# Optimization experiments

Hardware: AMD Instinct MI355X
Metric: run time of the kernel (lower is better)

## Reference

```python
import jax, jax.numpy as jnp
import numpy as np

B, C, N, K = 8, 128, 4096, 16
EPS = 1e-5


def _bn(x, g, b, m, v):
    # eval-mode BatchNorm1d over channel dim of [B, C, N]
    scale = (g * jax.lax.rsqrt(v + EPS))[None, :, None]
    return x * scale + (b - m * g * jax.lax.rsqrt(v + EPS))[None, :, None]


def setup_inputs() -> dict:
    key = jax.random.key(0)
    ks = jax.random.split(key, 16)
    x = jax.random.normal(ks[0], (B, C, N), dtype=jnp.float32)
    # k incoming neighbors per node, src within the same batch graph
    src_local = jax.random.randint(ks[1], (B, N, K), 0, N)
    src = (src_local + jnp.arange(B, dtype=src_local.dtype)[:, None, None] * N).reshape(B * N, K)
    def u(k, shape, lo, hi):
        return jax.random.uniform(k, shape, jnp.float32, lo, hi)
    params = dict(
        W1=jax.random.normal(ks[2], (C, C), jnp.float32) * (1.0 / np.sqrt(C)),
        b1=jax.random.normal(ks[3], (C,), jnp.float32) * 0.02,
        g1=u(ks[4], (C,), 0.5, 1.5), be1=jax.random.normal(ks[5], (C,)) * 0.1,
        m1=jax.random.normal(ks[6], (C,)) * 0.1, v1=u(ks[7], (C,), 0.5, 1.5),
        Wmr=jax.random.normal(ks[8], (2 * C, 2 * C), jnp.float32) * (1.0 / np.sqrt(2 * C)),
        bmr=jax.random.normal(ks[9], (2 * C,), jnp.float32) * 0.02,
        W2=jax.random.normal(ks[10], (C, 2 * C), jnp.float32) * (1.0 / np.sqrt(2 * C)),
        b2=jax.random.normal(ks[11], (C,), jnp.float32) * 0.02,
        g2=u(ks[12], (C,), 0.5, 1.5), be2=jax.random.normal(ks[13], (C,)) * 0.1,
        m2=jax.random.normal(ks[14], (C,)) * 0.1, v2=u(ks[15], (C,), 0.5, 1.5),
    )
    return {"x": x, "src": src, **params}


def reference(x, src, W1, b1, g1, be1, m1, v1, Wmr, bmr, W2, b2, g2, be2, m2, v2):
    res = x
    # fc1: Conv1d(k=1) + BN, then ReLU
    h = jnp.einsum('oc,bcn->bon', W1, x) + b1[None, :, None]
    h = jax.nn.relu(_bn(h, g1, be1, m1, v1))
    # nodes: [B*N, C]
    xn = h.transpose(0, 2, 1).reshape(B * N, C)
    # MRConv: max over incoming edges of (dst - src) feature diff
    diff = xn[:, None, :] - xn[src]          # [B*N, K, C]
    max_diff = diff.max(axis=1)              # [B*N, C]
    cat = jnp.concatenate([xn, max_diff], axis=1)  # [B*N, 2C]
    hn = jax.nn.relu(cat @ Wmr.T + bmr)      # [B*N, 2C]
    h2 = hn.reshape(B, N, 2 * C).transpose(0, 2, 1)  # [B, 2C, N]
    # fc2: Conv1d(k=1) + BN
    out = jnp.einsum('oc,bcn->bon', W2, h2) + b2[None, :, None]
    out = _bn(out, g2, be2, m2, v2)
    out = out + res
    return jax.nn.relu(out)
```

## Files before the change

### kernel.cpp

```cpp
#include <hip/hip_runtime.h>


typedef short bf8_t __attribute__((ext_vector_type(8)));
typedef float f4_t  __attribute__((ext_vector_type(4)));

namespace {
constexpr int Bn = 8, Cc = 128, Nn = 4096, Kk = 16, C2 = 256;
constexpr int NODES = Bn * Nn;
constexpr float EPSf = 1e-5f;
}

__device__ __forceinline__ unsigned short f2bf(float f) {
    unsigned u = __float_as_uint(f);
    u += 0x7fffu + ((u >> 16) & 1u);
    return (unsigned short)(u >> 16);
}
__device__ __forceinline__ unsigned pk2(float a, float b) {
    return (unsigned)f2bf(a) | ((unsigned)f2bf(b) << 16);
}
__device__ __forceinline__ float bflo(unsigned u) { return __uint_as_float(u << 16); }
__device__ __forceinline__ float bfhi(unsigned u) { return __uint_as_float(u & 0xffff0000u); }
__device__ __forceinline__ unsigned diff2(unsigned o, unsigned m) {
    return pk2(bflo(o) - bflo(m), bfhi(o) - bfhi(m));
}

__device__ __forceinline__ bf8_t cvt_frag(const float* __restrict__ p) {
    const float4 a = *(const float4*)(p);
    const float4 b = *(const float4*)(p + 4);
    union { uint4 u; bf8_t f; } r;
    r.u.x = pk2(a.x, a.y);
    r.u.y = pk2(a.z, a.w);
    r.u.z = pk2(b.x, b.y);
    r.u.w = pk2(b.z, b.w);
    return r.f;
}

#define PKMIN(a, b) asm("v_pk_min_u16 %0, %0, %1" : "+v"(a) : "v"(b))

__global__ __launch_bounds__(512) void fc1_mfma(
    const float* __restrict__ x, const float* __restrict__ W1,
    const float* __restrict__ b1, const float* __restrict__ g1,
    const float* __restrict__ be1, const float* __restrict__ m1,
    const float* __restrict__ v1, const float* __restrict__ Wmr,
    const float* __restrict__ W2, ushort* __restrict__ Wmrbf,
    ushort* __restrict__ W2bf, ushort* __restrict__ xn)
{
    __shared__ __align__(16) ushort xS[64 * 136];
    __shared__ float scS[Cc], shS[Cc];
    const int t = threadIdx.x;
    const int bid = blockIdx.x;

    if (bid < 96) {
        const int e = bid * 1024 + t * 2;
        if (e < 65536) {
            const float2 v = *(const float2*)(Wmr + e);
            *(unsigned*)(Wmrbf + e) = pk2(v.x, v.y);
        } else {
            const float2 v = *(const float2*)(W2 + (e - 65536));
            *(unsigned*)(W2bf + (e - 65536)) = pk2(v.x, v.y);
        }
    }

    const int lb = (bid & 7) * 64 + (bid >> 3);
    const int node0 = lb * 64;
    const int b  = node0 >> 12;
    const int n0 = node0 & 4095;

    if (t < Cc) {
        const float s = g1[t] * rsqrtf(v1[t] + EPSf);
        scS[t] = s;
        shS[t] = (b1[t] - m1[t]) * s + be1[t];
    }

    {
        const int cp = t >> 3, q = t & 7;
        const float* p0 = x + ((size_t)(b * Cc + 2 * cp)) * Nn + n0 + q * 8;
        const float* p1 = p0 + Nn;
        const float4 a0 = *(const float4*)(p0);
        const float4 a1 = *(const float4*)(p0 + 4);
        const float4 c0 = *(const float4*)(p1);
        const float4 c1 = *(const float4*)(p1 + 4);
        ushort* base = xS + (size_t)q * 8 * 136 + ((cp * 2) ^ (q << 3));
        *(unsigned*)(base + 0 * 136) = pk2(a0.x, c0.x);
        *(unsigned*)(base + 1 * 136) = pk2(a0.y, c0.y);
        *(unsigned*)(base + 2 * 136) = pk2(a0.z, c0.z);
        *(unsigned*)(base + 3 * 136) = pk2(a0.w, c0.w);
        *(unsigned*)(base + 4 * 136) = pk2(a1.x, c1.x);
        *(unsigned*)(base + 5 * 136) = pk2(a1.y, c1.y);
        *(unsigned*)(base + 6 * 136) = pk2(a1.z, c1.z);
        *(unsigned*)(base + 7 * 136) = pk2(a1.w, c1.w);
    }
    __syncthreads();

    const int w = t >> 6, lane = t & 63;
    const int row16 = lane & 15, kg = lane >> 4;

    f4_t acc[4];
    const f4_t zero = {0.f, 0.f, 0.f, 0.f};
    #pragma unroll
    for (int j = 0; j < 4; ++j) acc[j] = zero;

    #pragma unroll
    for (int ks = 0; ks < 4; ++ks) {
        const int k0 = ks * 32 + kg * 8;
        const bf8_t aw = cvt_frag(W1 + (size_t)(w * 16 + row16) * Cc + k0);
        #pragma unroll
        for (int nsub = 0; nsub < 4; ++nsub) {
            const int n = nsub * 16 + row16;
            const bf8_t bx = *(const bf8_t*)(xS + n * 136 + (k0 ^ ((n >> 3) << 3)));
            acc[nsub] = __builtin_amdgcn_mfma_f32_16x16x32_bf16(aw, bx, acc[nsub], 0, 0, 0);
        }
    }

    const int o4 = w * 16 + kg * 4;
    const float s0 = scS[o4 + 0], s1 = scS[o4 + 1], s2 = scS[o4 + 2], s3 = scS[o4 + 3];
    const float h0 = shS[o4 + 0], h1 = shS[o4 + 1], h2 = shS[o4 + 2], h3 = shS[o4 + 3];
    #pragma unroll
    for (int nsub = 0; nsub < 4; ++nsub) {
        const int node = node0 + nsub * 16 + row16;
        float v0 = acc[nsub][0] * s0 + h0;
        float v1 = acc[nsub][1] * s1 + h1;
        float v2 = acc[nsub][2] * s2 + h2;
        float v3 = acc[nsub][3] * s3 + h3;
        v0 = v0 > 0.f ? v0 : 0.f;
        v1 = v1 > 0.f ? v1 : 0.f;
        v2 = v2 > 0.f ? v2 : 0.f;
        v3 = v3 > 0.f ? v3 : 0.f;
        uint2 pk;
        pk.x = pk2(v0, v1);
        pk.y = pk2(v2, v3);
        *(uint2*)(xn + (size_t)node * Cc + o4) = pk;
    }
}

__global__ __launch_bounds__(512) void mrfc2_mfma(
    const ushort* __restrict__ xn, const int* __restrict__ src,
    const ushort* __restrict__ Wmrbf, const float* __restrict__ bmr,
    const ushort* __restrict__ W2bf, const float* __restrict__ x,
    const float* __restrict__ b2, const float* __restrict__ g2,
    const float* __restrict__ be2, const float* __restrict__ m2,
    const float* __restrict__ v2, float* __restrict__ out)
{
    __shared__ __align__(16) ushort catS[64 * 264];
    __shared__ __align__(16) float xresS[128 * 64];
    __shared__ float scS[Cc], shS[Cc];
    const int t = threadIdx.x;
    const int bid = blockIdx.x;
    const int lb = (bid & 7) * 64 + (bid >> 3);
    const int node0 = lb * 64;
    const int b  = node0 >> 12;
    const int n0 = node0 & 4095;

    const int xo = t >> 2, xseg = t & 3;
    const float* xsrc = x + ((size_t)(b * Cc + xo)) * Nn + n0 + xseg * 16;
    const float4 xr0 = ((const float4*)xsrc)[0];
    const float4 xr1 = ((const float4*)xsrc)[1];
    const float4 xr2 = ((const float4*)xsrc)[2];
    const float4 xr3 = ((const float4*)xsrc)[3];

    {
        const int nl = t >> 3, q = t & 7;
        const int node = node0 + nl;
        const int4 si0 = *(const int4*)(src + (size_t)node * Kk + 0);
        const int4 si1 = *(const int4*)(src + (size_t)node * Kk + 4);
        const int4 si2 = *(const int4*)(src + (size_t)node * Kk + 8);
        const int4 si3 = *(const int4*)(src + (size_t)node * Kk + 12);
        const int sl[16] = {si0.x, si0.y, si0.z, si0.w,
                            si1.x, si1.y, si1.z, si1.w,
                            si2.x, si2.y, si2.z, si2.w,
                            si3.x, si3.y, si3.z, si3.w};
        const ushort* orow = xn + (size_t)node * Cc + q * 16;
        uint4 ow0 = *(const uint4*)(orow + 0);
        uint4 ow1 = *(const uint4*)(orow + 8);
        const ushort* sr = xn + (size_t)sl[0] * Cc + q * 16;
        uint4 mn0 = *(const uint4*)(sr + 0);
        uint4 mn1 = *(const uint4*)(sr + 8);
        #pragma unroll
        for (int k = 1; k < Kk; ++k) {
            const ushort* s = xn + (size_t)sl[k] * Cc + q * 16;
            uint4 v0 = *(const uint4*)(s + 0);
            uint4 v1 = *(const uint4*)(s + 8);
            PKMIN(mn0.x, v0.x); PKMIN(mn0.y, v0.y); PKMIN(mn0.z, v0.z); PKMIN(mn0.w, v0.w);
            PKMIN(mn1.x, v1.x); PKMIN(mn1.y, v1.y); PKMIN(mn1.z, v1.z); PKMIN(mn1.w, v1.w);
        }
        unsigned* crow = (unsigned*)(catS + nl * 264);
        *(uint4*)(crow + q * 8 + 0) = ow0;
        *(uint4*)(crow + q * 8 + 4) = ow1;
        uint4 d0, d1;
        d0.x = diff2(ow0.x, mn0.x); d0.y = diff2(ow0.y, mn0.y);
        d0.z = diff2(ow0.z, mn0.z); d0.w = diff2(ow0.w, mn0.w);
        d1.x = diff2(ow1.x, mn1.x); d1.y = diff2(ow1.y, mn1.y);
        d1.z = diff2(ow1.z, mn1.z); d1.w = diff2(ow1.w, mn1.w);
        *(uint4*)(crow + 64 + q * 8 + 0) = d0;
        *(uint4*)(crow + 64 + q * 8 + 4) = d1;
    }

    {
        float* xd = xresS + xo * 64 + xseg * 16;
        ((float4*)xd)[0] = xr0;
        ((float4*)xd)[1] = xr1;
        ((float4*)xd)[2] = xr2;
        ((float4*)xd)[3] = xr3;
    }
    __syncthreads();

    const int w = t >> 6, lane = t & 63;
    const int row16 = lane & 15, kg = lane >> 4;

    const int jb = w * 32;
    {
        f4_t acc[2][4];
        const f4_t zero = {0.f, 0.f, 0.f, 0.f};
        #pragma unroll
        for (int i = 0; i < 2; ++i)
            #pragma unroll
            for (int j = 0; j < 4; ++j) acc[i][j] = zero;

        #pragma unroll
        for (int ks = 0; ks < 8; ++ks) {
            const int k0 = ks * 32 + kg * 8;
            bf8_t aw[2], bc[4];
            #pragma unroll
            for (int jsub = 0; jsub < 2; ++jsub)
                aw[jsub] = *(const bf8_t*)(Wmrbf + (size_t)(jb + jsub * 16 + row16) * C2 + k0);
            #pragma unroll
            for (int nsub = 0; nsub < 4; ++nsub)
                bc[nsub] = *(const bf8_t*)(catS + (nsub * 16 + row16) * 264 + k0);
            #pragma unroll
            for (int jsub = 0; jsub < 2; ++jsub)
                #pragma unroll
                for (int nsub = 0; nsub < 4; ++nsub)
                    acc[jsub][nsub] = __builtin_amdgcn_mfma_f32_16x16x32_bf16(
                        aw[jsub], bc[nsub], acc[jsub][nsub], 0, 0, 0);
        }

        if (t < Cc) {
            const float s = g2[t] * rsqrtf(v2[t] + EPSf);
            scS[t] = s;
            shS[t] = (b2[t] - m2[t]) * s + be2[t];
        }
        __syncthreads();

        #pragma unroll
        for (int jsub = 0; jsub < 2; ++jsub) {
            const float4 bb = *(const float4*)(bmr + jb + jsub * 16 + kg * 4);
            #pragma unroll
            for (int nsub = 0; nsub < 4; ++nsub) {
                float v0 = acc[jsub][nsub][0] + bb.x;
                float v1 = acc[jsub][nsub][1] + bb.y;
                float v2_ = acc[jsub][nsub][2] + bb.z;
                float v3 = acc[jsub][nsub][3] + bb.w;
                v0 = v0 > 0.f ? v0 : 0.f;
                v1 = v1 > 0.f ? v1 : 0.f;
                v2_ = v2_ > 0.f ? v2_ : 0.f;
                v3 = v3 > 0.f ? v3 : 0.f;
                uint2 pk;
                pk.x = pk2(v0, v1);
                pk.y = pk2(v2_, v3);
                *(uint2*)(catS + (nsub * 16 + row16) * 264 + jb + jsub * 16 + kg * 4) = pk;
            }
        }
    }
    __syncthreads();

    {
        const int ob = w * 16;
        f4_t acc[4];
        const f4_t zero = {0.f, 0.f, 0.f, 0.f};
        #pragma unroll
        for (int j = 0; j < 4; ++j) acc[j] = zero;

        #pragma unroll
        for (int ks = 0; ks < 8; ++ks) {
            const int k0 = ks * 32 + kg * 8;
            const bf8_t aw = *(const bf8_t*)(W2bf + (size_t)(ob + row16) * C2 + k0);
            #pragma unroll
            for (int nsub = 0; nsub < 4; ++nsub) {
                const bf8_t bh = *(const bf8_t*)(catS + (nsub * 16 + row16) * 264 + k0);
                acc[nsub] = __builtin_amdgcn_mfma_f32_16x16x32_bf16(aw, bh, acc[nsub], 0, 0, 0);
            }
        }

        #pragma unroll
        for (int r = 0; r < 4; ++r) {
            const int o = ob + kg * 4 + r;
            const float s = scS[o], sh = shS[o];
            const float* xl = xresS + o * 64;
            float*       op = out + ((size_t)(b * Cc + o)) * Nn + n0;
            #pragma unroll
            for (int nsub = 0; nsub < 4; ++nsub) {
                const int nn = nsub * 16 + row16;
                float v = acc[nsub][r] * s + sh + xl[nn];
                v = v > 0.f ? v : 0.f;
                op[nn] = v;
            }
        }
    }
}

extern "C" void kernel_launch(void* const* d_in, const int* in_sizes, int n_in,
                              void* d_out, int out_size, void* d_ws, size_t ws_size,
                              hipStream_t stream)
{
    const float* x   = (const float*)d_in[0];
    const int*   src = (const int*)  d_in[1];
    const float* W1  = (const float*)d_in[2];
    const float* b1  = (const float*)d_in[3];
    const float* g1  = (const float*)d_in[4];
    const float* be1 = (const float*)d_in[5];
    const float* m1  = (const float*)d_in[6];
    const float* v1  = (const float*)d_in[7];
    const float* Wmr = (const float*)d_in[8];
    const float* bmr = (const float*)d_in[9];
    const float* W2  = (const float*)d_in[10];
    const float* b2  = (const float*)d_in[11];
    const float* g2  = (const float*)d_in[12];
    const float* be2 = (const float*)d_in[13];
    const float* m2  = (const float*)d_in[14];
    const float* v2  = (const float*)d_in[15];
    float* out = (float*)d_out;

    ushort* Wmrbf = (ushort*)d_ws;
    ushort* W2bf  = Wmrbf + 65536;
    ushort* xn    = W2bf + 32768;

    fc1_mfma<<<NODES / 64, 512, 0, stream>>>(x, W1, b1, g1, be1, m1, v1,
                                             Wmr, W2, Wmrbf, W2bf, xn);
    mrfc2_mfma<<<NODES / 64, 512, 0, stream>>>(xn, src, Wmrbf, bmr, W2bf, x,
                                               b2, g2, be2, m2, v2, out);
}
```

Measured before the change: 35.63 us.

## Halve node tile in mrfc2 to 32 nodes with 256-thread blocks

The fused MRConv+fc2 kernel now processes 32 nodes per block with 4 waves instead of 64 nodes with 8 waves, doubling the grid. Each wave covers more output channels per node tile (64 for the MR GEMM, 32 for fc2), and the output write uses nontemporal stores. The smaller LDS footprint and block size should allow more blocks per CU and better latency hiding for the gather. In exchange, weight rows are reloaded twice as often per node, lowering weight reuse.

```diff
diff --git a/kernel.cpp b/kernel.cpp
--- a/kernel.cpp
+++ b/kernel.cpp
@@ -133,7 +133,7 @@
     }
 }
 
-__global__ __launch_bounds__(512) void mrfc2_mfma(
+__global__ __launch_bounds__(256) void mrfc2_mfma(
     const ushort* __restrict__ xn, const int* __restrict__ src,
     const ushort* __restrict__ Wmrbf, const float* __restrict__ bmr,
     const ushort* __restrict__ W2bf, const float* __restrict__ x,
@@ -141,17 +141,17 @@
     const float* __restrict__ be2, const float* __restrict__ m2,
     const float* __restrict__ v2, float* __restrict__ out)
 {
-    __shared__ __align__(16) ushort catS[64 * 264];
-    __shared__ __align__(16) float xresS[128 * 64];
+    __shared__ __align__(16) ushort catS[32 * 264];
+    __shared__ __align__(16) float xresS[128 * 32];
     __shared__ float scS[Cc], shS[Cc];
     const int t = threadIdx.x;
     const int bid = blockIdx.x;
-    const int lb = (bid & 7) * 64 + (bid >> 3);
-    const int node0 = lb * 64;
+    const int lb = (bid & 7) * 128 + (bid >> 3);
+    const int node0 = lb * 32;
     const int b  = node0 >> 12;
     const int n0 = node0 & 4095;
 
-    const int xo = t >> 2, xseg = t & 3;
+    const int xo = t >> 1, xseg = t & 1;
     const float* xsrc = x + ((size_t)(b * Cc + xo)) * Nn + n0 + xseg * 16;
     const float4 xr0 = ((const float4*)xsrc)[0];
     const float4 xr1 = ((const float4*)xsrc)[1];
@@ -196,7 +196,7 @@
     }
 
     {
-        float* xd = xresS + xo * 64 + xseg * 16;
+        float* xd = xresS + xo * 32 + xseg * 16;
         ((float4*)xd)[0] = xr0;
         ((float4*)xd)[1] = xr1;
         ((float4*)xd)[2] = xr2;
@@ -207,29 +207,29 @@
     const int w = t >> 6, lane = t & 63;
     const int row16 = lane & 15, kg = lane >> 4;
 
-    const int jb = w * 32;
-    {
-        f4_t acc[2][4];
+    const int jb = w * 64;
+    {
+        f4_t acc[4][2];
         const f4_t zero = {0.f, 0.f, 0.f, 0.f};
         #pragma unroll
-        for (int i = 0; i < 2; ++i)
-            #pragma unroll
-            for (int j = 0; j < 4; ++j) acc[i][j] = zero;
+        for (int i = 0; i < 4; ++i)
+            #pragma unroll
+            for (int j = 0; j < 2; ++j) acc[i][j] = zero;
 
         #pragma unroll
         for (int ks = 0; ks < 8; ++ks) {
             const int k0 = ks * 32 + kg * 8;
-            bf8_t aw[2], bc[4];
-            #pragma unroll
-            for (int jsub = 0; jsub < 2; ++jsub)
+            bf8_t aw[4], bc[2];
+            #pragma unroll
+            for (int jsub = 0; jsub < 4; ++jsub)
                 aw[jsub] = *(const bf8_t*)(Wmrbf + (size_t)(jb + jsub * 16 + row16) * C2 + k0);
             #pragma unroll
-            for (int nsub = 0; nsub < 4; ++nsub)
+            for (int nsub = 0; nsub < 2; ++nsub)
                 bc[nsub] = *(const bf8_t*)(catS + (nsub * 16 + row16) * 264 + k0);
             #pragma unroll
-            for (int jsub = 0; jsub < 2; ++jsub)
+            for (int jsub = 0; jsub < 4; ++jsub)
                 #pragma unroll
-                for (int nsub = 0; nsub < 4; ++nsub)
+                for (int nsub = 0; nsub < 2; ++nsub)
                     acc[jsub][nsub] = __builtin_amdgcn_mfma_f32_16x16x32_bf16(
                         aw[jsub], bc[nsub], acc[jsub][nsub], 0, 0, 0);
         }
@@ -242,10 +242,10 @@
         __syncthreads();
 
         #pragma unroll
-        for (int jsub = 0; jsub < 2; ++jsub) {
+        for (int jsub = 0; jsub < 4; ++jsub) {
             const float4 bb = *(const float4*)(bmr + jb + jsub * 16 + kg * 4);
             #pragma unroll
-            for (int nsub = 0; nsub < 4; ++nsub) {
+            for (int nsub = 0; nsub < 2; ++nsub) {
                 float v0 = acc[jsub][nsub][0] + bb.x;
                 float v1 = acc[jsub][nsub][1] + bb.y;
                 float v2_ = acc[jsub][nsub][2] + bb.z;
@@ -264,37 +264,48 @@
     __syncthreads();
 
     {
-        const int ob = w * 16;
-        f4_t acc[4];
+        const int ob = w * 32;
+        f4_t acc[2][2];
         const f4_t zero = {0.f, 0.f, 0.f, 0.f};
         #pragma unroll
-        for (int j = 0; j < 4; ++j) acc[j] = zero;
+        for (int i = 0; i < 2; ++i)
+            #pragma unroll
+            for (int j = 0; j < 2; ++j) acc[i][j] = zero;
 
         #pragma unroll
         for (int ks = 0; ks < 8; ++ks) {
             const int k0 = ks * 32 + kg * 8;
-            const bf8_t aw = *(const bf8_t*)(W2bf + (size_t)(ob + row16) * C2 + k0);
-            #pragma unroll
-            for (int nsub = 0; nsub < 4; ++nsub) {
-                const bf8_t bh = *(const bf8_t*)(catS + (nsub * 16 + row16) * 264 + k0);
-                acc[nsub] = __builtin_amdgcn_mfma_f32_16x16x32_bf16(aw, bh, acc[nsub], 0, 0, 0);
+            bf8_t aw[2], bh[2];
+            #pragma unroll
+            for (int osub = 0; osub < 2; ++osub)
+                aw[osub] = *(const bf8_t*)(W2bf + (size_t)(ob + osub * 16 + row16) * C2 + k0);
+            #pragma unroll
+            for (int nsub = 0; nsub < 2; ++nsub)
+                bh[nsub] = *(const bf8_t*)(catS + (nsub * 16 + row16) * 264 + k0);
+            #pragma unroll
+            for (int osub = 0; osub < 2; ++osub)
+                #pragma unroll
+                for (int nsub = 0; nsub < 2; ++nsub)
+                    acc[osub][nsub] = __builtin_amdgcn_mfma_f32_16x16x32_bf16(
+                        aw[osub], bh[nsub], acc[osub][nsub], 0, 0, 0);
+        }
+
+        #pragma unroll
+        for (int osub = 0; osub < 2; ++osub)
+            #pragma unroll
+            for (int r = 0; r < 4; ++r) {
+                const int o = ob + osub * 16 + kg * 4 + r;
+                const float s = scS[o], sh = shS[o];
+                const float* xl = xresS + o * 32;
+                float*       op = out + ((size_t)(b * Cc + o)) * Nn + n0;
+                #pragma unroll
+                for (int nsub = 0; nsub < 2; ++nsub) {
+                    const int nn = nsub * 16 + row16;
+                    float v = acc[osub][nsub][r] * s + sh + xl[nn];
+                    v = v > 0.f ? v : 0.f;
+                    __builtin_nontemporal_store(v, op + nn);
+                }
             }
-        }
-
-        #pragma unroll
-        for (int r = 0; r < 4; ++r) {
-            const int o = ob + kg * 4 + r;
-            const float s = scS[o], sh = shS[o];
-            const float* xl = xresS + o * 64;
-            float*       op = out + ((size_t)(b * Cc + o)) * Nn + n0;
-            #pragma unroll
-            for (int nsub = 0; nsub < 4; ++nsub) {
-                const int nn = nsub * 16 + row16;
-                float v = acc[nsub][r] * s + sh + xl[nn];
-                v = v > 0.f ? v : 0.f;
-                op[nn] = v;
-            }
-        }
     }
 }
 
@@ -326,6 +337,6 @@
 
     fc1_mfma<<<NODES / 64, 512, 0, stream>>>(x, W1, b1, g1, be1, m1, v1,
                                              Wmr, W2, Wmrbf, W2bf, xn);
-    mrfc2_mfma<<<NODES / 64, 512, 0, stream>>>(xn, src, Wmrbf, bmr, W2bf, x,
+    mrfc2_mfma<<<NODES / 32, 256, 0, stream>>>(xn, src, Wmrbf, bmr, W2bf, x,
                                                b2, g2, be2, m2, v2, out);
 }
```

After: 43.62 us. 1.22x slower.

## Overlap neighbor gather with first half of MR GEMM; drop residual LDS staging

Applied to the files above, without the earlier changes.

The fused MRConv+fc2 kernel now writes the center-node features to LDS first and runs the K=0..127 half of the Wmr MFMA while the 16-neighbor gather loads are in flight. The max-diff half is written afterwards and the second K half follows. The 32KB x-residual LDS buffer is removed and the residual is read directly from global memory in the epilogue. This cuts LDS use, which may raise occupancy, and hides gather latency behind MFMA work, at the cost of more live registers and uncoalesced-ish residual reads.

```diff
diff --git a/kernel.cpp b/kernel.cpp
--- a/kernel.cpp
+++ b/kernel.cpp
@@ -142,7 +142,6 @@
     const float* __restrict__ v2, float* __restrict__ out)
 {
     __shared__ __align__(16) ushort catS[64 * 264];
-    __shared__ __align__(16) float xresS[128 * 64];
     __shared__ float scS[Cc], shS[Cc];
     const int t = threadIdx.x;
     const int bid = blockIdx.x;
@@ -151,30 +150,36 @@
     const int b  = node0 >> 12;
     const int n0 = node0 & 4095;
 
-    const int xo = t >> 2, xseg = t & 3;
-    const float* xsrc = x + ((size_t)(b * Cc + xo)) * Nn + n0 + xseg * 16;
-    const float4 xr0 = ((const float4*)xsrc)[0];
-    const float4 xr1 = ((const float4*)xsrc)[1];
-    const float4 xr2 = ((const float4*)xsrc)[2];
-    const float4 xr3 = ((const float4*)xsrc)[3];
-
-    {
-        const int nl = t >> 3, q = t & 7;
-        const int node = node0 + nl;
-        const int4 si0 = *(const int4*)(src + (size_t)node * Kk + 0);
-        const int4 si1 = *(const int4*)(src + (size_t)node * Kk + 4);
-        const int4 si2 = *(const int4*)(src + (size_t)node * Kk + 8);
-        const int4 si3 = *(const int4*)(src + (size_t)node * Kk + 12);
+    const int w = t >> 6, lane = t & 63;
+    const int row16 = lane & 15, kg = lane >> 4;
+    const int jb = w * 32;
+
+    const int nl = t >> 3, q = t & 7;
+    const int node = node0 + nl;
+    const int4 si0 = *(const int4*)(src + (size_t)node * Kk + 0);
+    const int4 si1 = *(const int4*)(src + (size_t)node * Kk + 4);
+    const int4 si2 = *(const int4*)(src + (size_t)node * Kk + 8);
+    const int4 si3 = *(const int4*)(src + (size_t)node * Kk + 12);
+    const ushort* orow = xn + (size_t)node * Cc + q * 16;
+    const uint4 ow0 = *(const uint4*)(orow + 0);
+    const uint4 ow1 = *(const uint4*)(orow + 8);
+    {
+        unsigned* crow = (unsigned*)(catS + nl * 264);
+        *(uint4*)(crow + q * 8 + 0) = ow0;
+        *(uint4*)(crow + q * 8 + 4) = ow1;
+    }
+    __syncthreads();
+
+    uint4 mn0, mn1;
+    f4_t acc[2][4];
+    {
         const int sl[16] = {si0.x, si0.y, si0.z, si0.w,
                             si1.x, si1.y, si1.z, si1.w,
                             si2.x, si2.y, si2.z, si2.w,
                             si3.x, si3.y, si3.z, si3.w};
-        const ushort* orow = xn + (size_t)node * Cc + q * 16;
-        uint4 ow0 = *(const uint4*)(orow + 0);
-        uint4 ow1 = *(const uint4*)(orow + 8);
         const ushort* sr = xn + (size_t)sl[0] * Cc + q * 16;
-        uint4 mn0 = *(const uint4*)(sr + 0);
-        uint4 mn1 = *(const uint4*)(sr + 8);
+        mn0 = *(const uint4*)(sr + 0);
+        mn1 = *(const uint4*)(sr + 8);
         #pragma unroll
         for (int k = 1; k < Kk; ++k) {
             const ushort* s = xn + (size_t)sl[k] * Cc + q * 16;
@@ -183,92 +188,97 @@
             PKMIN(mn0.x, v0.x); PKMIN(mn0.y, v0.y); PKMIN(mn0.z, v0.z); PKMIN(mn0.w, v0.w);
             PKMIN(mn1.x, v1.x); PKMIN(mn1.y, v1.y); PKMIN(mn1.z, v1.z); PKMIN(mn1.w, v1.w);
         }
-        unsigned* crow = (unsigned*)(catS + nl * 264);
-        *(uint4*)(crow + q * 8 + 0) = ow0;
-        *(uint4*)(crow + q * 8 + 4) = ow1;
+
+        const f4_t zero = {0.f, 0.f, 0.f, 0.f};
+        #pragma unroll
+        for (int i = 0; i < 2; ++i)
+            #pragma unroll
+            for (int j = 0; j < 4; ++j) acc[i][j] = zero;
+
+        const ushort* wr0 = Wmrbf + (size_t)(jb + row16) * C2;
+        const ushort* wr1 = Wmrbf + (size_t)(jb + 16 + row16) * C2;
+        #pragma unroll
+        for (int ks = 0; ks < 4; ++ks) {
+            const int k0 = ks * 32 + kg * 8;
+            const bf8_t aw0 = *(const bf8_t*)(wr0 + k0);
+            const bf8_t aw1 = *(const bf8_t*)(wr1 + k0);
+            bf8_t bc[4];
+            #pragma unroll
+            for (int nsub = 0; nsub < 4; ++nsub)
+                bc[nsub] = *(const bf8_t*)(catS + (nsub * 16 + row16) * 264 + k0);
+            #pragma unroll
+            for (int nsub = 0; nsub < 4; ++nsub) {
+                acc[0][nsub] = __builtin_amdgcn_mfma_f32_16x16x32_bf16(aw0, bc[nsub], acc[0][nsub], 0, 0, 0);
+                acc[1][nsub] = __builtin_amdgcn_mfma_f32_16x16x32_bf16(aw1, bc[nsub], acc[1][nsub], 0, 0, 0);
+            }
+        }
+    }
+
+    {
         uint4 d0, d1;
         d0.x = diff2(ow0.x, mn0.x); d0.y = diff2(ow0.y, mn0.y);
         d0.z = diff2(ow0.z, mn0.z); d0.w = diff2(ow0.w, mn0.w);
         d1.x = diff2(ow1.x, mn1.x); d1.y = diff2(ow1.y, mn1.y);
         d1.z = diff2(ow1.z, mn1.z); d1.w = diff2(ow1.w, mn1.w);
+        unsigned* crow = (unsigned*)(catS + nl * 264);
         *(uint4*)(crow + 64 + q * 8 + 0) = d0;
         *(uint4*)(crow + 64 + q * 8 + 4) = d1;
     }
-
-    {
-        float* xd = xresS + xo * 64 + xseg * 16;
-        ((float4*)xd)[0] = xr0;
-        ((float4*)xd)[1] = xr1;
-        ((float4*)xd)[2] = xr2;
-        ((float4*)xd)[3] = xr3;
-    }
-    __syncthreads();
-
-    const int w = t >> 6, lane = t & 63;
-    const int row16 = lane & 15, kg = lane >> 4;
-
-    const int jb = w * 32;
-    {
-        f4_t acc[2][4];
-        const f4_t zero = {0.f, 0.f, 0.f, 0.f};
-        #pragma unroll
-        for (int i = 0; i < 2; ++i)
-            #pragma unroll
-            for (int j = 0; j < 4; ++j) acc[i][j] = zero;
-
-        #pragma unroll
-        for (int ks = 0; ks < 8; ++ks) {
+    if (t < Cc) {
+        const float s = g2[t] * rsqrtf(v2[t] + EPSf);
+        scS[t] = s;
+        shS[t] = (b2[t] - m2[t]) * s + be2[t];
+    }
+    __syncthreads();
+
+    {
+        const ushort* wr0 = Wmrbf + (size_t)(jb + row16) * C2;
+        const ushort* wr1 = Wmrbf + (size_t)(jb + 16 + row16) * C2;
+        #pragma unroll
+        for (int ks = 4; ks < 8; ++ks) {
             const int k0 = ks * 32 + kg * 8;
-            bf8_t aw[2], bc[4];
-            #pragma unroll
-            for (int jsub = 0; jsub < 2; ++jsub)
-                aw[jsub] = *(const bf8_t*)(Wmrbf + (size_t)(jb + jsub * 16 + row16) * C2 + k0);
+            const bf8_t aw0 = *(const bf8_t*)(wr0 + k0);
+            const bf8_t aw1 = *(const bf8_t*)(wr1 + k0);
+            bf8_t bc[4];
             #pragma unroll
             for (int nsub = 0; nsub < 4; ++nsub)
                 bc[nsub] = *(const bf8_t*)(catS + (nsub * 16 + row16) * 264 + k0);
             #pragma unroll
-            for (int jsub = 0; jsub < 2; ++jsub)
-                #pragma unroll
-                for (int nsub = 0; nsub < 4; ++nsub)
-                    acc[jsub][nsub] = __builtin_amdgcn_mfma_f32_16x16x32_bf16(
-                        aw[jsub], bc[nsub], acc[jsub][nsub], 0, 0, 0);
-        }
-
-        if (t < Cc) {
-            const float s = g2[t] * rsqrtf(v2[t] + EPSf);
-            scS[t] = s;
-            shS[t] = (b2[t] - m2[t]) * s + be2[t];
-        }
-        __syncthreads();
-
-        #pragma unroll
-        for (int jsub = 0; jsub < 2; ++jsub) {
-            const float4 bb = *(const float4*)(bmr + jb + jsub * 16 + kg * 4);
-            #pragma unroll
             for (int nsub = 0; nsub < 4; ++nsub) {
-                float v0 = acc[jsub][nsub][0] + bb.x;
-                float v1 = acc[jsub][nsub][1] + bb.y;
-                float v2_ = acc[jsub][nsub][2] + bb.z;
-                float v3 = acc[jsub][nsub][3] + bb.w;
-                v0 = v0 > 0.f ? v0 : 0.f;
-                v1 = v1 > 0.f ? v1 : 0.f;
-                v2_ = v2_ > 0.f ? v2_ : 0.f;
-                v3 = v3 > 0.f ? v3 : 0.f;
-                uint2 pk;
-                pk.x = pk2(v0, v1);
-                pk.y = pk2(v2_, v3);
-                *(uint2*)(catS + (nsub * 16 + row16) * 264 + jb + jsub * 16 + kg * 4) = pk;
+                acc[0][nsub] = __builtin_amdgcn_mfma_f32_16x16x32_bf16(aw0, bc[nsub], acc[0][nsub], 0, 0, 0);
+                acc[1][nsub] = __builtin_amdgcn_mfma_f32_16x16x32_bf16(aw1, bc[nsub], acc[1][nsub], 0, 0, 0);
             }
         }
     }
     __syncthreads();
 
+    #pragma unroll
+    for (int jsub = 0; jsub < 2; ++jsub) {
+        const float4 bb = *(const float4*)(bmr + jb + jsub * 16 + kg * 4);
+        #pragma unroll
+        for (int nsub = 0; nsub < 4; ++nsub) {
+            float v0 = acc[jsub][nsub][0] + bb.x;
+            float v1 = acc[jsub][nsub][1] + bb.y;
+            float v2_ = acc[jsub][nsub][2] + bb.z;
+            float v3 = acc[jsub][nsub][3] + bb.w;
+            v0 = v0 > 0.f ? v0 : 0.f;
+            v1 = v1 > 0.f ? v1 : 0.f;
+            v2_ = v2_ > 0.f ? v2_ : 0.f;
+            v3 = v3 > 0.f ? v3 : 0.f;
+            uint2 pk;
+            pk.x = pk2(v0, v1);
+            pk.y = pk2(v2_, v3);
+            *(uint2*)(catS + (nsub * 16 + row16) * 264 + jb + jsub * 16 + kg * 4) = pk;
+        }
+    }
+    __syncthreads();
+
     {
         const int ob = w * 16;
-        f4_t acc[4];
+        f4_t acc3[4];
         const f4_t zero = {0.f, 0.f, 0.f, 0.f};
         #pragma unroll
-        for (int j = 0; j < 4; ++j) acc[j] = zero;
+        for (int j = 0; j < 4; ++j) acc3[j] = zero;
 
         #pragma unroll
         for (int ks = 0; ks < 8; ++ks) {
@@ -277,7 +287,7 @@
             #pragma unroll
             for (int nsub = 0; nsub < 4; ++nsub) {
                 const bf8_t bh = *(const bf8_t*)(catS + (nsub * 16 + row16) * 264 + k0);
-                acc[nsub] = __builtin_amdgcn_mfma_f32_16x16x32_bf16(aw, bh, acc[nsub], 0, 0, 0);
+                acc3[nsub] = __builtin_amdgcn_mfma_f32_16x16x32_bf16(aw, bh, acc3[nsub], 0, 0, 0);
             }
         }
 
@@ -285,12 +295,12 @@
         for (int r = 0; r < 4; ++r) {
             const int o = ob + kg * 4 + r;
             const float s = scS[o], sh = shS[o];
-            const float* xl = xresS + o * 64;
+            const float* xr = x   + ((size_t)(b * Cc + o)) * Nn + n0;
             float*       op = out + ((size_t)(b * Cc + o)) * Nn + n0;
             #pragma unroll
             for (int nsub = 0; nsub < 4; ++nsub) {
                 const int nn = nsub * 16 + row16;
-                float v = acc[nsub][r] * s + sh + xl[nn];
+                float v = acc3[nsub][r] * s + sh + xr[nn];
                 v = v > 0.f ? v : 0.f;
                 op[nn] = v;
             }
```

New measurement: 37.12 us. 4.2% more time.
